# Kernel optimization log

Hardware: AMD Instinct MI355X
Metric: run time of the kernel (lower is better)

Reference implementation:

```python
import jax, jax.numpy as jnp
import numpy as np

N = 50000      # nodes
E = 800000     # edges (before self-loops)
F_IN = 64      # num_features
HID = 32       # hidden_channels
HEADS = 4
CLS = 3
NEG_SLOPE = 0.2  # PyG GATConv default


def setup_inputs() -> dict:
    key = jax.random.key(0)
    ks = jax.random.split(key, 12)
    s = 0.1
    return {
        "x": jax.random.normal(ks[0], (N, F_IN), jnp.float32),
        "W1": jax.random.normal(ks[1], (F_IN, HEADS * HID), jnp.float32) * s,
        "att_src1": jax.random.normal(ks[2], (HEADS, HID), jnp.float32) * s,
        "att_dst1": jax.random.normal(ks[3], (HEADS, HID), jnp.float32) * s,
        "b1": jnp.zeros((HEADS * HID,), jnp.float32),
        "W2": jax.random.normal(ks[4], (HEADS * HID, HID), jnp.float32) * s,
        "att_src2": jax.random.normal(ks[5], (1, HID), jnp.float32) * s,
        "att_dst2": jax.random.normal(ks[6], (1, HID), jnp.float32) * s,
        "b2": jnp.zeros((HID,), jnp.float32),
        "linW": jax.random.normal(ks[7], (HID, CLS), jnp.float32) * s,
        "linb": jnp.zeros((CLS,), jnp.float32),
        "edge_index": jax.random.randint(ks[8], (2, E), 0, N, dtype=jnp.int64),
    }


def _gat_conv(x, W, att_src, att_dst, bias, src, dst, heads):
    """PyG GATConv (eval mode, self-loops pre-added in src/dst)."""
    n = x.shape[0]
    h = (x @ W).reshape(n, heads, -1)                      # [N,H,C]
    a_src = jnp.sum(h * att_src, axis=-1)                  # [N,H]
    a_dst = jnp.sum(h * att_dst, axis=-1)                  # [N,H]
    e = jax.nn.leaky_relu(a_src[src] + a_dst[dst], NEG_SLOPE)  # [E,H]
    # segment softmax over destination node
    m = jax.ops.segment_max(e, dst, num_segments=n)
    p = jnp.exp(e - m[dst])
    denom = jax.ops.segment_sum(p, dst, num_segments=n)
    alpha = p / denom[dst]                                 # [E,H]
    msg = h[src] * alpha[:, :, None]                       # [E,H,C]
    out = jax.ops.segment_sum(msg, dst, num_segments=n)    # [N,H,C]
    return out.reshape(n, -1) + bias                       # concat heads


def reference(x, W1, att_src1, att_dst1, b1, W2, att_src2, att_dst2, b2, linW, linb, edge_index):
    n = x.shape[0]
    loop = jnp.arange(n, dtype=edge_index.dtype)
    src = jnp.concatenate([edge_index[0], loop])  # add self-loops (PyG default)
    dst = jnp.concatenate([edge_index[1], loop])
    h = _gat_conv(x, W1, att_src1, att_dst1, b1, src, dst, HEADS)
    h = jax.nn.elu(h)
    h = _gat_conv(h, W2, att_src2, att_dst2, b2, src, dst, 1)
    g = jnp.mean(h, axis=0, keepdims=True)        # batch is None path
    logits = g @ linW + linb                      # [1, CLS]
    return jax.nn.softmax(logits, axis=1)
```

## Files before the change

kernel.cpp:

```cpp
#include <hip/hip_runtime.h>
#include <hip/hip_fp16.h>
#include <math.h>

#define NEG_SLOPE 0.2f
#define CAP 64

static __device__ __forceinline__ void atomAdd(float* a, float v) {
    unsafeAtomicAdd(a, v);
}

static __device__ __forceinline__ bool edges_are_i64(const int* __restrict__ ei) {
    return (ei[1] | ei[3] | ei[5] | ei[7]) == 0;
}
static __device__ __forceinline__ int ldsrc(const int* __restrict__ ei, int e, int E, bool i64) {
    return i64 ? ei[2 * e] : ei[e];
}
static __device__ __forceinline__ int lddst(const int* __restrict__ ei, int e, int E, bool i64) {
    return i64 ? ei[2 * (E + e)] : ei[E + e];
}

__global__ void scatter_k(const int* __restrict__ ei, int* __restrict__ deg,
                          int* __restrict__ col, int E, int N) {
    int e = blockIdx.x * blockDim.x + threadIdx.x;
    if (e >= E + N) return;
    bool i64 = edges_are_i64(ei);
    int s, d;
    if (e < E) { s = ldsrc(ei, e, E, i64); d = lddst(ei, e, E, i64); }
    else       { s = d = e - E; }
    int pos = atomicAdd(&deg[d], 1);
    if (pos < CAP) col[d * CAP + pos] = s;
}

__global__ __launch_bounds__(256, 4) void gemm1_k(const float* __restrict__ x,
                                                  const float* __restrict__ W,
                                                  const float* __restrict__ aws,
                                                  const float* __restrict__ awd,
                                                  __half* __restrict__ h,
                                                  float* __restrict__ as_,
                                                  float* __restrict__ ad_, int N) {
    __shared__ float Ws[64 * 128];
    __shared__ float xs[32 * 64];
    const int tid = threadIdx.x;
    const int cg = tid & 31, rg = tid >> 5;
    const int r0 = blockIdx.x * 32;
#pragma unroll 1
    for (int i = tid; i < 8192; i += 256) Ws[i] = W[i];
    {
        const float* src = x + (size_t)r0 * 64;
        const int limit = (N - r0) * 64;
#pragma unroll 1
        for (int i = tid * 4; i < 2048; i += 1024) {
            float4 v = (i < limit) ? *(const float4*)(src + i) : make_float4(0, 0, 0, 0);
            *(float4*)(xs + i) = v;
        }
    }
    __syncthreads();

    float acc[4][4] = {};
#pragma unroll 2
    for (int k = 0; k < 64; k += 4) {
        float4 w0 = *(const float4*)(Ws + (k + 0) * 128 + cg * 4);
        float4 w1 = *(const float4*)(Ws + (k + 1) * 128 + cg * 4);
        float4 w2 = *(const float4*)(Ws + (k + 2) * 128 + cg * 4);
        float4 w3 = *(const float4*)(Ws + (k + 3) * 128 + cg * 4);
        float4 xv[4];
#pragma unroll
        for (int q = 0; q < 4; ++q) xv[q] = *(const float4*)(xs + (rg * 4 + q) * 64 + k);
#pragma unroll
        for (int q = 0; q < 4; ++q) {
            float4 xq = xv[q];
            acc[q][0] += xq.x * w0.x + xq.y * w1.x + xq.z * w2.x + xq.w * w3.x;
            acc[q][1] += xq.x * w0.y + xq.y * w1.y + xq.z * w2.y + xq.w * w3.y;
            acc[q][2] += xq.x * w0.z + xq.y * w1.z + xq.z * w2.z + xq.w * w3.z;
            acc[q][3] += xq.x * w0.w + xq.y * w1.w + xq.z * w2.w + xq.w * w3.w;
        }
    }

    const int jbase = cg * 4;
    const int head = cg >> 3;
    const float a0 = aws[jbase], a1 = aws[jbase + 1], a2 = aws[jbase + 2], a3 = aws[jbase + 3];
    const float d0 = awd[jbase], d1 = awd[jbase + 1], d2 = awd[jbase + 2], d3 = awd[jbase + 3];
    float ps[4], pd[4];
#pragma unroll
    for (int q = 0; q < 4; ++q) {
        ps[q] = acc[q][0] * a0 + acc[q][1] * a1 + acc[q][2] * a2 + acc[q][3] * a3;
        pd[q] = acc[q][0] * d0 + acc[q][1] * d1 + acc[q][2] * d2 + acc[q][3] * d3;
        int row = r0 + rg * 4 + q;
        if (row < N) {
            __half hv[4];
            hv[0] = __float2half(acc[q][0]); hv[1] = __float2half(acc[q][1]);
            hv[2] = __float2half(acc[q][2]); hv[3] = __float2half(acc[q][3]);
            *(uint2*)(h + (size_t)row * 128 + jbase) = *(uint2*)hv;
        }
    }
#pragma unroll
    for (int off = 4; off; off >>= 1) {
#pragma unroll
        for (int q = 0; q < 4; ++q) {
            ps[q] += __shfl_down(ps[q], off, 8);
            pd[q] += __shfl_down(pd[q], off, 8);
        }
    }
    if ((cg & 7) == 0) {
#pragma unroll
        for (int q = 0; q < 4; ++q) {
            int row = r0 + rg * 4 + q;
            if (row < N) { as_[row * 4 + head] = ps[q]; ad_[row * 4 + head] = pd[q]; }
        }
    }
}

__global__ __launch_bounds__(256, 4) void gemm2_k(const float* __restrict__ hact,
                                                  const float* __restrict__ W,
                                                  const float* __restrict__ aws,
                                                  const float* __restrict__ awd,
                                                  __half* __restrict__ h2,
                                                  float* __restrict__ as_,
                                                  float* __restrict__ ad_, int N) {
    __shared__ float Ws[128 * 32];
    __shared__ float xs[128 * 68];
    const int tid = threadIdx.x;
    const int cg = tid & 7, rg = tid >> 3;
    const int r0 = blockIdx.x * 128;
    for (int i = tid; i < 4096; i += 256) Ws[i] = W[i];

    float acc[4][4] = {};
#pragma unroll 1
    for (int p = 0; p < 2; ++p) {
        __syncthreads();
#pragma unroll 2
        for (int i = tid * 4; i < 8192; i += 1024) {
            int row = i >> 6, kk = i & 63;
            float4 v = (r0 + row < N)
                ? *(const float4*)(hact + (size_t)(r0 + row) * 128 + p * 64 + kk)
                : make_float4(0, 0, 0, 0);
            *(float4*)(xs + row * 68 + kk) = v;
        }
        __syncthreads();
#pragma unroll 2
        for (int k = 0; k < 64; k += 4) {
            float4 w0 = *(const float4*)(Ws + (p * 64 + k + 0) * 32 + cg * 4);
            float4 w1 = *(const float4*)(Ws + (p * 64 + k + 1) * 32 + cg * 4);
            float4 w2 = *(const float4*)(Ws + (p * 64 + k + 2) * 32 + cg * 4);
            float4 w3 = *(const float4*)(Ws + (p * 64 + k + 3) * 32 + cg * 4);
            float4 xv[4];
#pragma unroll
            for (int q = 0; q < 4; ++q) xv[q] = *(const float4*)(xs + (rg * 4 + q) * 68 + k);
#pragma unroll
            for (int q = 0; q < 4; ++q) {
                float4 xq = xv[q];
                acc[q][0] += xq.x * w0.x + xq.y * w1.x + xq.z * w2.x + xq.w * w3.x;
                acc[q][1] += xq.x * w0.y + xq.y * w1.y + xq.z * w2.y + xq.w * w3.y;
                acc[q][2] += xq.x * w0.z + xq.y * w1.z + xq.z * w2.z + xq.w * w3.z;
                acc[q][3] += xq.x * w0.w + xq.y * w1.w + xq.z * w2.w + xq.w * w3.w;
            }
        }
    }

    const int jbase = cg * 4;
    const float a0 = aws[jbase], a1 = aws[jbase + 1], a2 = aws[jbase + 2], a3 = aws[jbase + 3];
    const float d0 = awd[jbase], d1 = awd[jbase + 1], d2 = awd[jbase + 2], d3 = awd[jbase + 3];
    float ps[4], pd[4];
#pragma unroll
    for (int q = 0; q < 4; ++q) {
        ps[q] = acc[q][0] * a0 + acc[q][1] * a1 + acc[q][2] * a2 + acc[q][3] * a3;
        pd[q] = acc[q][0] * d0 + acc[q][1] * d1 + acc[q][2] * d2 + acc[q][3] * d3;
        int row = r0 + rg * 4 + q;
        if (row < N) {
            __half hv[4];
            hv[0] = __float2half(acc[q][0]); hv[1] = __float2half(acc[q][1]);
            hv[2] = __float2half(acc[q][2]); hv[3] = __float2half(acc[q][3]);
            *(uint2*)(h2 + (size_t)row * 32 + jbase) = *(uint2*)hv;
        }
    }
#pragma unroll
    for (int off = 4; off; off >>= 1) {
#pragma unroll
        for (int q = 0; q < 4; ++q) {
            ps[q] += __shfl_down(ps[q], off, 8);
            pd[q] += __shfl_down(pd[q], off, 8);
        }
    }
    if (cg == 0) {
#pragma unroll
        for (int q = 0; q < 4; ++q) {
            int row = r0 + rg * 4 + q;
            if (row < N) { as_[row] = ps[q]; ad_[row] = pd[q]; }
        }
    }
}

__global__ __launch_bounds__(256) void pull_agg1_k(const int* __restrict__ deg,
                                                   const int* __restrict__ col,
                                                   const float* __restrict__ asrc,
                                                   const float* __restrict__ adst,
                                                   const __half* __restrict__ h,
                                                   const float* __restrict__ b1,
                                                   float* __restrict__ hact, int N) {
    int wave = (blockIdx.x * 256 + threadIdx.x) >> 6;
    int lane = threadIdx.x & 63;
    if (wave >= N) return;
    const int d = wave;
    const int hd = lane >> 4;
    const float ad = adst[d * 4 + hd];
    const int* cl = col + d * CAP;
    int cnt = deg[d]; if (cnt > CAP) cnt = CAP;
    float acc0 = 0.0f, acc1 = 0.0f, den = 0.0f;
    int i = 0;
    for (; i + 8 <= cnt; i += 8) {
        int s[8]; float v[8]; __half2 g[8];
#pragma unroll
        for (int u = 0; u < 8; ++u) s[u] = cl[i + u];
#pragma unroll
        for (int u = 0; u < 8; ++u) v[u] = asrc[s[u] * 4 + hd] + ad;
#pragma unroll
        for (int u = 0; u < 8; ++u) g[u] = *(const __half2*)(h + (size_t)s[u] * 128 + lane * 2);
#pragma unroll
        for (int u = 0; u < 8; ++u) {
            float vv = v[u] > 0.0f ? v[u] : NEG_SLOPE * v[u];
            float p = __expf(vv);
            float2 gf = __half22float2(g[u]);
            den += p; acc0 += p * gf.x; acc1 += p * gf.y;
        }
    }
    for (; i < cnt; ++i) {
        int s = cl[i];
        float v = asrc[s * 4 + hd] + ad;
        v = v > 0.0f ? v : NEG_SLOPE * v;
        float p = __expf(v);
        float2 gf = __half22float2(*(const __half2*)(h + (size_t)s * 128 + lane * 2));
        den += p; acc0 += p * gf.x; acc1 += p * gf.y;
    }
    float inv = 1.0f / den;
    float o0 = acc0 * inv + b1[lane * 2];
    float o1 = acc1 * inv + b1[lane * 2 + 1];
    o0 = o0 > 0.0f ? o0 : expm1f(o0);
    o1 = o1 > 0.0f ? o1 : expm1f(o1);
    *(float2*)(hact + (size_t)d * 128 + lane * 2) = make_float2(o0, o1);
}

__global__ __launch_bounds__(256) void pull_agg2_k(const int* __restrict__ deg,
                                                   const int* __restrict__ col,
                                                   const float* __restrict__ asrc,
                                                   const float* __restrict__ adst,
                                                   const __half* __restrict__ h,
                                                   float* __restrict__ out, int N) {
    int grp = (blockIdx.x * 256 + threadIdx.x) >> 5;
    int lane = threadIdx.x & 31;
    if (grp >= N) return;
    const int d = grp;
    const float ad = adst[d];
    const int* cl = col + d * CAP;
    int cnt = deg[d]; if (cnt > CAP) cnt = CAP;
    float acc = 0.0f, den = 0.0f;
    int i = 0;
    for (; i + 8 <= cnt; i += 8) {
        int s[8]; float v[8]; __half g[8];
#pragma unroll
        for (int u = 0; u < 8; ++u) s[u] = cl[i + u];
#pragma unroll
        for (int u = 0; u < 8; ++u) v[u] = asrc[s[u]] + ad;
#pragma unroll
        for (int u = 0; u < 8; ++u) g[u] = h[(size_t)s[u] * 32 + lane];
#pragma unroll
        for (int u = 0; u < 8; ++u) {
            float vv = v[u] > 0.0f ? v[u] : NEG_SLOPE * v[u];
            float p = __expf(vv);
            den += p; acc += p * __half2float(g[u]);
        }
    }
    for (; i < cnt; ++i) {
        int s = cl[i];
        float v = asrc[s] + ad;
        v = v > 0.0f ? v : NEG_SLOPE * v;
        float p = __expf(v);
        den += p; acc += p * __half2float(h[(size_t)s * 32 + lane]);
    }
    out[(size_t)d * 32 + lane] = acc / den;
}

__global__ __launch_bounds__(256) void colmean_k(const float* __restrict__ out2,
                                                 float* __restrict__ gsum, int N) {
    __shared__ float lds[256];
    int tid = threadIdx.x;
    int c = tid % 32;
    int rg = tid / 32;
    float acc = 0.0f;
    for (int r = blockIdx.x * 8 + rg; r < N; r += gridDim.x * 8)
        acc += out2[(size_t)r * 32 + c];
    lds[tid] = acc;
    __syncthreads();
    if (tid < 32) {
        float s = 0.0f;
#pragma unroll
        for (int g = 0; g < 8; ++g) s += lds[g * 32 + tid];
        atomAdd(&gsum[tid], s);
    }
}

__global__ void final_k(const float* __restrict__ gsum, const float* __restrict__ b2w,
                        const float* __restrict__ linW, const float* __restrict__ linb,
                        float* __restrict__ out, int N) {
    if (threadIdx.x != 0 || blockIdx.x != 0) return;
    float g[32];
#pragma unroll
    for (int c = 0; c < 32; ++c) g[c] = gsum[c] / (float)N + b2w[c];
    float lo[3];
#pragma unroll
    for (int j = 0; j < 3; ++j) {
        float acc = linb[j];
#pragma unroll
        for (int c = 0; c < 32; ++c) acc += g[c] * linW[c * 3 + j];
        lo[j] = acc;
    }
    float mx = fmaxf(lo[0], fmaxf(lo[1], lo[2]));
    float ex[3], se = 0.0f;
#pragma unroll
    for (int j = 0; j < 3; ++j) { ex[j] = __expf(lo[j] - mx); se += ex[j]; }
#pragma unroll
    for (int j = 0; j < 3; ++j) out[j] = ex[j] / se;
}

extern "C" void kernel_launch(void* const* d_in, const int* in_sizes, int n_in,
                              void* d_out, int out_size, void* d_ws, size_t ws_size,
                              hipStream_t stream) {
    const float* x    = (const float*)d_in[0];
    const float* W1   = (const float*)d_in[1];
    const float* as1w = (const float*)d_in[2];
    const float* ad1w = (const float*)d_in[3];
    const float* b1   = (const float*)d_in[4];
    const float* W2   = (const float*)d_in[5];
    const float* as2w = (const float*)d_in[6];
    const float* ad2w = (const float*)d_in[7];
    const float* b2w  = (const float*)d_in[8];
    const float* linW = (const float*)d_in[9];
    const float* linb = (const float*)d_in[10];
    const int*   ei   = (const int*)d_in[11];

    const int N  = in_sizes[0] / 64;
    const int E  = in_sizes[11] / 2;
    const int ET = E + N;

    float* ws = (float*)d_ws;
    __half* h1h  = (__half*)ws;
    float*  hact = ws + (size_t)N * 64;
    float* asrc1 = hact + (size_t)N * 128;
    float* adst1 = asrc1 + (size_t)N * 4;
    float* asrc2 = adst1 + (size_t)N * 4;
    float* adst2 = asrc2 + (size_t)N;
    float* gsum  = adst2 + (size_t)N;
    __half* h2h  = (__half*)ws;
    float*  out2 = ws + (size_t)N * 16;
    int* deg     = (int*)(gsum + 32);
    int* col     = deg + N;

    auto cdiv = [](int a, int b) { return (a + b - 1) / b; };

    hipMemsetAsync(deg, 0, (size_t)N * sizeof(int), stream);
    hipMemsetAsync(gsum, 0, 32 * sizeof(float), stream);

    scatter_k<<<cdiv(ET, 256), 256, 0, stream>>>(ei, deg, col, E, N);

    gemm1_k<<<cdiv(N, 32), 256, 0, stream>>>(x, W1, as1w, ad1w, h1h, asrc1, adst1, N);
    pull_agg1_k<<<cdiv(N, 4), 256, 0, stream>>>(deg, col, asrc1, adst1, h1h, b1, hact, N);

    gemm2_k<<<cdiv(N, 128), 256, 0, stream>>>(hact, W2, as2w, ad2w, h2h, asrc2, adst2, N);
    pull_agg2_k<<<cdiv(N, 8), 256, 0, stream>>>(deg, col, asrc2, adst2, h2h, out2, N);

    colmean_k<<<256, 256, 0, stream>>>(out2, gsum, N);
    final_k<<<1, 64, 0, stream>>>(gsum, b2w, linW, linb, (float*)d_out, N);
}
```

Baseline: 268.9 us.

## Fuse edge scatter and first-layer GEMM into one block-partitioned kernel

Merges the CSR-building scatter kernel and the layer-1 GEMM into a single launch with 2048 blocks: the first half grid-stride over edges doing atomic degree counting, the second half loop persistently over 32-row tiles, loading W1 into shared memory once per block. This removes one kernel launch, lets the atomic-bound scatter overlap with the compute-bound GEMM, and amortizes the W1 shared-memory load across tiles. In exchange, each half gets a fixed share of the grid, so load imbalance is possible, and occupancy for the scatter blocks is limited by the GEMM's shared-memory footprint.

```diff
diff --git a/kernel.cpp b/kernel.cpp
--- a/kernel.cpp
+++ b/kernel.cpp
@@ -19,93 +19,109 @@
     return i64 ? ei[2 * (E + e)] : ei[E + e];
 }
 
-__global__ void scatter_k(const int* __restrict__ ei, int* __restrict__ deg,
-                          int* __restrict__ col, int E, int N) {
-    int e = blockIdx.x * blockDim.x + threadIdx.x;
-    if (e >= E + N) return;
-    bool i64 = edges_are_i64(ei);
-    int s, d;
-    if (e < E) { s = ldsrc(ei, e, E, i64); d = lddst(ei, e, E, i64); }
-    else       { s = d = e - E; }
-    int pos = atomicAdd(&deg[d], 1);
-    if (pos < CAP) col[d * CAP + pos] = s;
-}
-
-__global__ __launch_bounds__(256, 4) void gemm1_k(const float* __restrict__ x,
-                                                  const float* __restrict__ W,
+__global__ __launch_bounds__(256, 4) void fuseA_k(const int* __restrict__ ei,
+                                                  int* __restrict__ deg,
+                                                  int* __restrict__ col,
+                                                  const float* __restrict__ x,
+                                                  const float* __restrict__ W1,
                                                   const float* __restrict__ aws,
                                                   const float* __restrict__ awd,
                                                   __half* __restrict__ h,
                                                   float* __restrict__ as_,
-                                                  float* __restrict__ ad_, int N) {
-    __shared__ float Ws[64 * 128];
-    __shared__ float xs[32 * 64];
+                                                  float* __restrict__ ad_,
+                                                  int E, int N) {
+    __shared__ float smem[10240];
     const int tid = threadIdx.x;
-    const int cg = tid & 31, rg = tid >> 5;
-    const int r0 = blockIdx.x * 32;
+    const int nScat = gridDim.x >> 1;
+
+    if (blockIdx.x < nScat) {
+        const bool i64 = edges_are_i64(ei);
+        const int ET = E + N;
+        for (int e = blockIdx.x * 256 + tid; e < ET; e += nScat * 256) {
+            int s, d;
+            if (e < E) { s = ldsrc(ei, e, E, i64); d = lddst(ei, e, E, i64); }
+            else       { s = d = e - E; }
+            int pos = atomicAdd(&deg[d], 1);
+            if (pos < CAP) col[d * CAP + pos] = s;
+        }
+        return;
+    }
+
+    float* Ws = smem;
+    float* xs = smem + 8192;
+    const int cgi = tid & 31, rg = tid >> 5;
+    const int nG = gridDim.x - nScat;
+    const int tiles = (N + 31) / 32;
 #pragma unroll 1
-    for (int i = tid; i < 8192; i += 256) Ws[i] = W[i];
-    {
-        const float* src = x + (size_t)r0 * 64;
-        const int limit = (N - r0) * 64;
-#pragma unroll 1
-        for (int i = tid * 4; i < 2048; i += 1024) {
-            float4 v = (i < limit) ? *(const float4*)(src + i) : make_float4(0, 0, 0, 0);
-            *(float4*)(xs + i) = v;
-        }
-    }
-    __syncthreads();
-
-    float acc[4][4] = {};
-#pragma unroll 2
-    for (int k = 0; k < 64; k += 4) {
-        float4 w0 = *(const float4*)(Ws + (k + 0) * 128 + cg * 4);
-        float4 w1 = *(const float4*)(Ws + (k + 1) * 128 + cg * 4);
-        float4 w2 = *(const float4*)(Ws + (k + 2) * 128 + cg * 4);
-        float4 w3 = *(const float4*)(Ws + (k + 3) * 128 + cg * 4);
-        float4 xv[4];
-#pragma unroll
-        for (int q = 0; q < 4; ++q) xv[q] = *(const float4*)(xs + (rg * 4 + q) * 64 + k);
-#pragma unroll
-        for (int q = 0; q < 4; ++q) {
-            float4 xq = xv[q];
-            acc[q][0] += xq.x * w0.x + xq.y * w1.x + xq.z * w2.x + xq.w * w3.x;
-            acc[q][1] += xq.x * w0.y + xq.y * w1.y + xq.z * w2.y + xq.w * w3.y;
-            acc[q][2] += xq.x * w0.z + xq.y * w1.z + xq.z * w2.z + xq.w * w3.z;
-            acc[q][3] += xq.x * w0.w + xq.y * w1.w + xq.z * w2.w + xq.w * w3.w;
-        }
-    }
-
-    const int jbase = cg * 4;
-    const int head = cg >> 3;
+    for (int i = tid; i < 8192; i += 256) Ws[i] = W1[i];
+
+    const int jbase = cgi * 4;
+    const int head = cgi >> 3;
     const float a0 = aws[jbase], a1 = aws[jbase + 1], a2 = aws[jbase + 2], a3 = aws[jbase + 3];
     const float d0 = awd[jbase], d1 = awd[jbase + 1], d2 = awd[jbase + 2], d3 = awd[jbase + 3];
-    float ps[4], pd[4];
-#pragma unroll
-    for (int q = 0; q < 4; ++q) {
-        ps[q] = acc[q][0] * a0 + acc[q][1] * a1 + acc[q][2] * a2 + acc[q][3] * a3;
-        pd[q] = acc[q][0] * d0 + acc[q][1] * d1 + acc[q][2] * d2 + acc[q][3] * d3;
-        int row = r0 + rg * 4 + q;
-        if (row < N) {
-            __half hv[4];
-            hv[0] = __float2half(acc[q][0]); hv[1] = __float2half(acc[q][1]);
-            hv[2] = __float2half(acc[q][2]); hv[3] = __float2half(acc[q][3]);
-            *(uint2*)(h + (size_t)row * 128 + jbase) = *(uint2*)hv;
-        }
-    }
-#pragma unroll
-    for (int off = 4; off; off >>= 1) {
+
+#pragma unroll 1
+    for (int t = blockIdx.x - nScat; t < tiles; t += nG) {
+        const int r0 = t * 32;
+        __syncthreads();
+        {
+            const float* src = x + (size_t)r0 * 64;
+            const int limit = (N - r0) * 64;
+#pragma unroll 1
+            for (int i = tid * 4; i < 2048; i += 1024) {
+                float4 v = (i < limit) ? *(const float4*)(src + i) : make_float4(0, 0, 0, 0);
+                *(float4*)(xs + i) = v;
+            }
+        }
+        __syncthreads();
+
+        float acc[4][4] = {};
+#pragma unroll 2
+        for (int k = 0; k < 64; k += 4) {
+            float4 w0 = *(const float4*)(Ws + (k + 0) * 128 + cgi * 4);
+            float4 w1 = *(const float4*)(Ws + (k + 1) * 128 + cgi * 4);
+            float4 w2 = *(const float4*)(Ws + (k + 2) * 128 + cgi * 4);
+            float4 w3 = *(const float4*)(Ws + (k + 3) * 128 + cgi * 4);
+            float4 xv[4];
+#pragma unroll
+            for (int q = 0; q < 4; ++q) xv[q] = *(const float4*)(xs + (rg * 4 + q) * 64 + k);
+#pragma unroll
+            for (int q = 0; q < 4; ++q) {
+                float4 xq = xv[q];
+                acc[q][0] += xq.x * w0.x + xq.y * w1.x + xq.z * w2.x + xq.w * w3.x;
+                acc[q][1] += xq.x * w0.y + xq.y * w1.y + xq.z * w2.y + xq.w * w3.y;
+                acc[q][2] += xq.x * w0.z + xq.y * w1.z + xq.z * w2.z + xq.w * w3.z;
+                acc[q][3] += xq.x * w0.w + xq.y * w1.w + xq.z * w2.w + xq.w * w3.w;
+            }
+        }
+
+        float ps[4], pd[4];
 #pragma unroll
         for (int q = 0; q < 4; ++q) {
-            ps[q] += __shfl_down(ps[q], off, 8);
-            pd[q] += __shfl_down(pd[q], off, 8);
-        }
-    }
-    if ((cg & 7) == 0) {
-#pragma unroll
-        for (int q = 0; q < 4; ++q) {
+            ps[q] = acc[q][0] * a0 + acc[q][1] * a1 + acc[q][2] * a2 + acc[q][3] * a3;
+            pd[q] = acc[q][0] * d0 + acc[q][1] * d1 + acc[q][2] * d2 + acc[q][3] * d3;
             int row = r0 + rg * 4 + q;
-            if (row < N) { as_[row * 4 + head] = ps[q]; ad_[row * 4 + head] = pd[q]; }
+            if (row < N) {
+                __half hv[4];
+                hv[0] = __float2half(acc[q][0]); hv[1] = __float2half(acc[q][1]);
+                hv[2] = __float2half(acc[q][2]); hv[3] = __float2half(acc[q][3]);
+                *(uint2*)(h + (size_t)row * 128 + jbase) = *(uint2*)hv;
+            }
+        }
+#pragma unroll
+        for (int off = 4; off; off >>= 1) {
+#pragma unroll
+            for (int q = 0; q < 4; ++q) {
+                ps[q] += __shfl_down(ps[q], off, 8);
+                pd[q] += __shfl_down(pd[q], off, 8);
+            }
+        }
+        if ((cgi & 7) == 0) {
+#pragma unroll
+            for (int q = 0; q < 4; ++q) {
+                int row = r0 + rg * 4 + q;
+                if (row < N) { as_[row * 4 + head] = ps[q]; ad_[row * 4 + head] = pd[q]; }
+            }
         }
     }
 }
@@ -337,9 +353,8 @@
     const float* linb = (const float*)d_in[10];
     const int*   ei   = (const int*)d_in[11];
 
-    const int N  = in_sizes[0] / 64;
-    const int E  = in_sizes[11] / 2;
-    const int ET = E + N;
+    const int N = in_sizes[0] / 64;
+    const int E = in_sizes[11] / 2;
 
     float* ws = (float*)d_ws;
     __half* h1h  = (__half*)ws;
@@ -359,9 +374,9 @@
     hipMemsetAsync(deg, 0, (size_t)N * sizeof(int), stream);
     hipMemsetAsync(gsum, 0, 32 * sizeof(float), stream);
 
-    scatter_k<<<cdiv(ET, 256), 256, 0, stream>>>(ei, deg, col, E, N);
-
-    gemm1_k<<<cdiv(N, 32), 256, 0, stream>>>(x, W1, as1w, ad1w, h1h, asrc1, adst1, N);
+    fuseA_k<<<2048, 256, 0, stream>>>(ei, deg, col, x, W1, as1w, ad1w,
+                                      h1h, asrc1, adst1, E, N);
+
     pull_agg1_k<<<cdiv(N, 4), 256, 0, stream>>>(deg, col, asrc1, adst1, h1h, b1, hact, N);
 
     gemm2_k<<<cdiv(N, 128), 256, 0, stream>>>(hact, W2, as2w, ad2w, h2h, asrc2, adst2, N);
```

Measured after the change: 270.0 us. About the same (+0.4%).
